# Optimization experiments

Measured on AMD Instinct MI355X. Metric: run time of the kernel, lower is better.

The kernel has to match this reference:

```python
import jax, jax.numpy as jnp
import numpy as np

N_NODES = 2000
N_FEAT = 16
HID = 64
RNN_LAYERS = 2
OUT_WIN = 24
OUT_DIM = 1
N_Q = 3
LN_EPS = 1e-5


def _layernorm(x, g, b):
    mu = jnp.mean(x, axis=-1, keepdims=True)
    var = jnp.mean((x - mu) ** 2, axis=-1, keepdims=True)
    return (x - mu) * jax.lax.rsqrt(var + LN_EPS) * g + b


def setup_inputs() -> dict:
    key = jax.random.key(0)
    ks = jax.random.split(key, 24)
    B, S, N, F, H = 4, 96, N_NODES, N_FEAT, HID
    E = 16000
    inp = {}
    inp['x'] = jax.random.normal(ks[0], (B, S, N, F), dtype=jnp.float32)
    inp['edge_index'] = jax.random.randint(ks[1], (2, E), 0, N, dtype=jnp.int64)
    inp['edge_weight'] = jax.random.uniform(ks[2], (E,), dtype=jnp.float32)
    sc = 1.0 / np.sqrt(H)
    inp['W_gcn'] = jax.random.normal(ks[3], (H, F)) * (1.0 / np.sqrt(F))
    inp['b_gcn'] = jnp.zeros((H,))
    inp['Wq'] = jax.random.normal(ks[4], (H, H)) * sc
    inp['Wk'] = jax.random.normal(ks[5], (H, H)) * sc
    inp['Wv'] = jax.random.normal(ks[6], (H, H)) * sc
    inp['v_w'] = jax.random.normal(ks[7], (1, H)) * sc
    inp['v_b'] = jnp.zeros((1,))
    inp['ln1_g'] = jnp.ones((H,)); inp['ln1_b'] = jnp.zeros((H,))
    inp['gru_Wih'] = jax.random.normal(ks[8], (RNN_LAYERS, 3 * H, H)) * sc
    inp['gru_Whh'] = jax.random.normal(ks[9], (RNN_LAYERS, 3 * H, H)) * sc
    inp['gru_bih'] = jnp.zeros((RNN_LAYERS, 3 * H))
    inp['gru_bhh'] = jnp.zeros((RNN_LAYERS, 3 * H))
    inp['ln2_g'] = jnp.ones((H,)); inp['ln2_b'] = jnp.zeros((H,))
    inp['pre1_W'] = jax.random.normal(ks[10], (2 * H, H)) * sc
    inp['pre1_b'] = jnp.zeros((2 * H,))
    inp['pre2_W'] = jax.random.normal(ks[11], (N * H, 2 * H)) * (1.0 / np.sqrt(2 * H))
    inp['pre2_b'] = jnp.zeros((N * H,))
    inp['low_W'] = jax.random.normal(ks[12], (OUT_WIN * OUT_DIM, H)) * sc
    inp['low_b'] = jnp.zeros((OUT_WIN * OUT_DIM,))
    inp['inc_W'] = jax.random.normal(ks[13], (OUT_WIN * OUT_DIM * (N_Q - 1), H)) * sc
    inp['inc_b'] = jnp.zeros((OUT_WIN * OUT_DIM * (N_Q - 1),))
    return inp


def reference(x, edge_index, edge_weight, W_gcn, b_gcn, Wq, Wk, Wv, v_w, v_b,
              ln1_g, ln1_b, gru_Wih, gru_Whh, gru_bih, gru_bhh, ln2_g, ln2_b,
              pre1_W, pre1_b, pre2_W, pre2_b, low_W, low_b, inc_W, inc_b):
    B, S, N, F = x.shape
    H = W_gcn.shape[0]
    # ---- GCNConv (PyG semantics: add self-loops, symmetric normalization) ----
    # Graph is identical across batch/timesteps, so vectorize the per-timestep
    # loop into one batched gather/scatter.
    src, dst = edge_index[0], edge_index[1]
    loops = jnp.arange(N, dtype=edge_index.dtype)
    src_a = jnp.concatenate([src, loops])
    dst_a = jnp.concatenate([dst, loops])
    ew_a = jnp.concatenate([edge_weight, jnp.ones((N,), dtype=edge_weight.dtype)])
    deg = jax.ops.segment_sum(ew_a, dst_a, num_segments=N)
    dinv = jnp.where(deg > 0, deg ** -0.5, 0.0)
    coef = dinv[src_a] * ew_a * dinv[dst_a]  # (E+N,)
    xw = jnp.einsum('bsnf,hf->bsnh', x, W_gcn)  # linear (no bias yet)
    msg = xw[:, :, src_a, :] * coef[None, None, :, None]  # (B,S,E+N,H)
    h = jnp.zeros((B, S, N, H), dtype=xw.dtype).at[:, :, dst_a].add(msg)
    h = jax.nn.elu(h + b_gcn)  # dropout is identity in eval
    # ---- additive attention over all (t, node) positions ----
    keys = h.reshape(B, S * N, H)
    query = h[:, -1].mean(axis=1)  # (B,H)
    qp = query @ Wq.T  # (B,H)
    kp = keys @ Wk.T   # (B,SN,H)
    vp = keys @ Wv.T
    energy = jnp.tanh(qp[:, None, :] + kp)
    scores = energy @ v_w[0] + v_b[0]  # (B,SN)
    attn = jax.nn.softmax(scores, axis=1)
    context = jnp.einsum('bk,bkh->bh', attn, vp)
    context = _layernorm(context, ln1_g, ln1_b)
    # ---- GRU with seq_len=1, h0=0 (torch gate order: r,z,n) ----
    inp = context
    for l in range(gru_Wih.shape[0]):
        gi = inp @ gru_Wih[l].T + gru_bih[l]  # (B,3H)
        gh = gru_bhh[l]                        # h_prev = 0
        i_r, i_z, i_n = jnp.split(gi, 3, axis=-1)
        h_r, h_z, h_n = jnp.split(gh, 3, axis=-1)
        r = jax.nn.sigmoid(i_r + h_r)
        z = jax.nn.sigmoid(i_z + h_z)
        n = jnp.tanh(i_n + r * h_n)
        inp = (1.0 - z) * n  # + z * 0
    final = _layernorm(inp, ln2_g, ln2_b)
    # ---- pre_head -> per-node features ----
    f = jax.nn.elu(final @ pre1_W.T + pre1_b)
    nf = (f @ pre2_W.T + pre2_b).reshape(B, N, H)
    # ---- monotonic quantile head ----
    q_low = (nf @ low_W.T + low_b).reshape(B, N, OUT_WIN, OUT_DIM)
    inc = jax.nn.softplus((nf @ inc_W.T + inc_b).reshape(B, N, OUT_WIN, OUT_DIM, N_Q - 1))
    q1 = q_low + inc[..., 0]
    q2 = q1 + inc[..., 1]
    quant = jnp.stack([q_low, q1, q2], axis=-1)  # (B,N,OW,OD,Q)
    predictions = jnp.transpose(quant, (0, 2, 1, 3, 4))  # (B,OW,N,OD,Q)
    return predictions, attn.reshape(B, S, N)
```

## Files before the change

### kernel.cpp

```cpp
#include <hip/hip_runtime.h>

#define B 4
#define S 96
#define NN 2000
#define FF 16
#define HH 64
#define EE 16000
#define SN (S*NN)
#define SLICES (B*S)
#define BSN (B*SN)
#define KB_TOTAL (BSN/16)
#define KB_PER_B (SN/16)
#define OUT_PRED (B*24*NN*3)

typedef __attribute__((ext_vector_type(8))) short short8;
typedef __attribute__((ext_vector_type(4))) float f32x4;

__device__ __forceinline__ unsigned short f2bf(float f){
  unsigned u = __float_as_uint(f);
  u += 0x7fffu + ((u >> 16) & 1u);
  return (unsigned short)(u >> 16);
}
__device__ __forceinline__ float bf2f(unsigned short s){
  return __uint_as_float(((unsigned)s) << 16);
}
__device__ __forceinline__ float fast_tanh(float x){
  float e = __builtin_amdgcn_exp2f(x * 2.8853900817779268f);
  return 1.0f - 2.0f * __builtin_amdgcn_rcpf(e + 1.0f);
}
__device__ __forceinline__ float sigm(float x){ return 1.0f / (1.0f + __expf(-x)); }
__device__ __forceinline__ float eluf(float x){ return x > 0.0f ? x : expm1f(x); }
__device__ __forceinline__ float softplusf_(float x){
  return fmaxf(x, 0.0f) + log1pf(__expf(-fabsf(x)));
}

__global__ void k_pinit(float* __restrict__ degw, int* __restrict__ cnt){
  int i = blockIdx.x * 256 + threadIdx.x;
  if (i < NN){ degw[i] = 1.0f; cnt[i] = 1; }
}

__global__ void k_deg(const int* __restrict__ ei, const float* __restrict__ ew,
                      float* __restrict__ degw, int* __restrict__ cnt){
  int e = blockIdx.x * 256 + threadIdx.x;
  if (e < EE){
    int d = ei[EE + e];
    atomicAdd(&degw[d], ew[e]);
    atomicAdd(&cnt[d], 1);
  }
}

__global__ void k_scan(const int* __restrict__ cnt, float* __restrict__ degw,
                       int* __restrict__ rowptr, int* __restrict__ curs){
  __shared__ int tsum[256];
  int tid = threadIdx.x;
  for (int i = tid; i < NN; i += 256){
    float deg = degw[i];
    degw[i] = deg > 0.0f ? rsqrtf(deg) : 0.0f;
  }
  int base = tid * 8;
  int loc[8]; int s = 0;
  #pragma unroll
  for (int j = 0; j < 8; ++j){
    int v = (base + j < NN) ? cnt[base + j] : 0;
    loc[j] = s; s += v;
  }
  tsum[tid] = s;
  __syncthreads();
  for (int off = 1; off < 256; off <<= 1){
    int v = (tid >= off) ? tsum[tid - off] : 0;
    __syncthreads();
    tsum[tid] += v;
    __syncthreads();
  }
  int excl = tsum[tid] - s;
  #pragma unroll
  for (int j = 0; j < 8; ++j)
    if (base + j < NN){ rowptr[base + j] = excl + loc[j]; curs[base + j] = excl + loc[j]; }
  if (tid == 0) rowptr[NN] = EE + NN;
}

__global__ void k_fill(const int* __restrict__ ei, const float* __restrict__ ew,
                       const float* __restrict__ dinv, int* __restrict__ curs,
                       uint2* __restrict__ epack){
  int e = blockIdx.x * 256 + threadIdx.x;
  if (e < EE){
    int s0 = ei[e], d = ei[EE + e];
    int pos = atomicAdd(&curs[d], 1);
    epack[pos] = make_uint2((unsigned)s0, __float_as_uint(dinv[s0] * ew[e] * dinv[d]));
  }
  int i = blockIdx.x * 256 + threadIdx.x;
  if (i < NN){
    int pos = atomicAdd(&curs[i], 1);
    epack[pos] = make_uint2((unsigned)i, __float_as_uint(dinv[i] * dinv[i]));
  }
}

__global__ __launch_bounds__(512) void k_agg(const float* __restrict__ x,
    const int* __restrict__ rowptr, const uint2* __restrict__ epack,
    unsigned* __restrict__ aggG){
  __shared__ unsigned xs[2][NN * 4];
  int tid = threadIdx.x;
  int spair = blockIdx.x >> 1;
  int halfF = blockIdx.x & 1;
  int s0 = spair * 2;

  #pragma unroll
  for (int ss = 0; ss < 2; ++ss){
    const float* xg = x + (size_t)(s0 + ss) * (NN * FF) + halfF * 8;
    for (int i = tid; i < 4000; i += 512){
      int n = i >> 1, p = i & 1;
      float4 v = *(const float4*)(xg + n * 16 + p * 4);
      xs[ss][n * 4 + p * 2]     = (unsigned)f2bf(v.x) | ((unsigned)f2bf(v.y) << 16);
      xs[ss][n * 4 + p * 2 + 1] = (unsigned)f2bf(v.z) | ((unsigned)f2bf(v.w) << 16);
    }
  }
  __syncthreads();

  int rs[4], re[4];
  #pragma unroll
  for (int g = 0; g < 4; ++g){
    int n = g * 512 + tid;
    if (n < NN){ rs[g] = rowptr[n]; re[g] = rowptr[n + 1]; }
    else { rs[g] = 0; re[g] = 0; }
  }
  float agg[4][2][8];
  #pragma unroll
  for (int g = 0; g < 4; ++g)
    #pragma unroll
    for (int ss = 0; ss < 2; ++ss)
      #pragma unroll
      for (int i = 0; i < 8; ++i) agg[g][ss][i] = 0.0f;

  #pragma unroll
  for (int g = 0; g < 4; ++g){
    for (int e = rs[g]; e < re[g]; ++e){
      uint2 m = epack[e];
      int s = (int)m.x;
      float c = __uint_as_float(m.y);
      uint4 u0 = *(const uint4*)&xs[0][s * 4];
      uint4 u1 = *(const uint4*)&xs[1][s * 4];
      agg[g][0][0] += c * __uint_as_float(u0.x << 16);
      agg[g][0][1] += c * __uint_as_float(u0.x & 0xffff0000u);
      agg[g][0][2] += c * __uint_as_float(u0.y << 16);
      agg[g][0][3] += c * __uint_as_float(u0.y & 0xffff0000u);
      agg[g][0][4] += c * __uint_as_float(u0.z << 16);
      agg[g][0][5] += c * __uint_as_float(u0.z & 0xffff0000u);
      agg[g][0][6] += c * __uint_as_float(u0.w << 16);
      agg[g][0][7] += c * __uint_as_float(u0.w & 0xffff0000u);
      agg[g][1][0] += c * __uint_as_float(u1.x << 16);
      agg[g][1][1] += c * __uint_as_float(u1.x & 0xffff0000u);
      agg[g][1][2] += c * __uint_as_float(u1.y << 16);
      agg[g][1][3] += c * __uint_as_float(u1.y & 0xffff0000u);
      agg[g][1][4] += c * __uint_as_float(u1.z << 16);
      agg[g][1][5] += c * __uint_as_float(u1.z & 0xffff0000u);
      agg[g][1][6] += c * __uint_as_float(u1.w << 16);
      agg[g][1][7] += c * __uint_as_float(u1.w & 0xffff0000u);
    }
  }
  #pragma unroll
  for (int g = 0; g < 4; ++g){
    int n = g * 512 + tid;
    if (n < NN){
      #pragma unroll
      for (int ss = 0; ss < 2; ++ss){
        unsigned u[4];
        #pragma unroll
        for (int j = 0; j < 4; ++j)
          u[j] = (unsigned)f2bf(agg[g][ss][2*j]) | ((unsigned)f2bf(agg[g][ss][2*j+1]) << 16);
        uint4* dst = (uint4*)(aggG + ((size_t)(s0 + ss) * NN + n) * 8 + halfF * 4);
        *dst = make_uint4(u[0], u[1], u[2], u[3]);
      }
    }
  }
}

__global__ __launch_bounds__(256) void k_xform(const unsigned short* __restrict__ aggG,
    const float* __restrict__ Wg, const float* __restrict__ bg,
    unsigned short* __restrict__ h){
  int lane = threadIdx.x & 63;
  int wid  = threadIdx.x >> 6;
  int wgid = blockIdx.x * 4 + wid;
  int row16 = lane & 15, half = lane >> 4;

  short8 bf[4];
  #pragma unroll
  for (int t = 0; t < 4; ++t){
    short8 v;
    #pragma unroll
    for (int j = 0; j < 8; ++j) v[j] = 0;
    if (half < 2){
      const float* wr = Wg + (t * 16 + row16) * 16 + half * 8;
      #pragma unroll
      for (int j = 0; j < 8; ++j) v[j] = (short)f2bf(wr[j]);
    }
    bf[t] = v;
  }
  float bias[4];
  #pragma unroll
  for (int t = 0; t < 4; ++t) bias[t] = bg[t * 16 + row16];

  for (int nb = wgid; nb < KB_TOTAL; nb += 8192){
    short8 af;
    #pragma unroll
    for (int j = 0; j < 8; ++j) af[j] = 0;
    if (half < 2)
      af = *(const short8*)(aggG + ((size_t)nb * 16 + row16) * 16 + half * 8);

    f32x4 acc[4];
    #pragma unroll
    for (int t = 0; t < 4; ++t){
      f32x4 a = {0.f, 0.f, 0.f, 0.f};
      acc[t] = __builtin_amdgcn_mfma_f32_16x16x32_bf16(af, bf[t], a, 0, 0, 0);
    }
    unsigned short* hp = h + (size_t)nb * 16 * 64;
    #pragma unroll
    for (int t = 0; t < 4; ++t){
      #pragma unroll
      for (int r = 0; r < 4; ++r){
        float v = acc[t][r] + bias[t];
        float e = v > 0.0f ? v : __expf(v) - 1.0f;
        hp[(half * 4 + r) * 64 + t * 16 + row16] = f2bf(e);
      }
    }
  }
}

__global__ void k_query(const unsigned short* __restrict__ h,
                        const float* __restrict__ Wq, float* __restrict__ qp){
  __shared__ float part[256];
  __shared__ float q[64];
  int b = blockIdx.x, tid = threadIdx.x;
  int i = tid & 63, chunk = tid >> 6;
  const unsigned short* hb = h + ((size_t)(b * S + (S - 1)) * NN) * HH;
  float p = 0.0f;
  for (int n = chunk * 500; n < chunk * 500 + 500; ++n) p += bf2f(hb[n * HH + i]);
  part[tid] = p;
  __syncthreads();
  if (tid < 64) q[tid] = (part[tid] + part[tid+64] + part[tid+128] + part[tid+192]) * (1.0f / NN);
  __syncthreads();
  if (tid < 64){
    float acc = 0.0f;
    for (int k = 0; k < 64; ++k) acc += q[k] * Wq[tid * 64 + k];
    qp[b * 64 + tid] = acc;
  }
}

__global__ __launch_bounds__(256) void k_scores(const unsigned short* __restrict__ h,
    const float* __restrict__ Wk, const float* __restrict__ vw,
    const float* __restrict__ qp, float* __restrict__ scores){
  int lane = threadIdx.x & 63;
  int wid = threadIdx.x >> 6;
  int wgid = blockIdx.x * 4 + wid;
  int row16 = lane & 15, half = lane >> 4;

  short8 bf[4][2];
  #pragma unroll
  for (int t = 0; t < 4; ++t){
    int n = 16 * t + row16;
    #pragma unroll
    for (int s2 = 0; s2 < 2; ++s2){
      const float* wr = Wk + n * 64 + 32 * s2 + half * 8;
      short8 v;
      #pragma unroll
      for (int j = 0; j < 8; ++j) v[j] = (short)f2bf(wr[j]);
      bf[t][s2] = v;
    }
  }
  float vwv[4];
  #pragma unroll
  for (int t = 0; t < 4; ++t) vwv[t] = vw[16 * t + row16];

  int b = wgid / 2000;
  float qv[4];
  #pragma unroll
  for (int t = 0; t < 4; ++t) qv[t] = qp[b * 64 + 16 * t + row16];

  int kb0 = wgid * 6;
  #pragma unroll 2
  for (int i = 0; i < 6; ++i){
    int kb = kb0 + i;
    const short* hp = (const short*)h + (size_t)kb * 16 * 64;
    short8 af[2];
    #pragma unroll
    for (int s2 = 0; s2 < 2; ++s2)
      af[s2] = *(const short8*)(hp + row16 * 64 + 32 * s2 + half * 8);

    f32x4 acc[4];
    #pragma unroll
    for (int t = 0; t < 4; ++t){
      f32x4 a = {0.f, 0.f, 0.f, 0.f};
      a = __builtin_amdgcn_mfma_f32_16x16x32_bf16(af[0], bf[t][0], a, 0, 0, 0);
      a = __builtin_amdgcn_mfma_f32_16x16x32_bf16(af[1], bf[t][1], a, 0, 0, 0);
      acc[t] = a;
    }
    float part[4] = {0, 0, 0, 0};
    #pragma unroll
    for (int t = 0; t < 4; ++t){
      #pragma unroll
      for (int r = 0; r < 4; ++r)
        part[r] += vwv[t] * fast_tanh(qv[t] + acc[t][r]);
    }
    #pragma unroll
    for (int r = 0; r < 4; ++r){
      part[r] += __shfl_xor(part[r], 1);
      part[r] += __shfl_xor(part[r], 2);
      part[r] += __shfl_xor(part[r], 4);
      part[r] += __shfl_xor(part[r], 8);
    }
    if (row16 == 0){
      #pragma unroll
      for (int r = 0; r < 4; ++r) scores[kb * 16 + half * 4 + r] = part[r];
    }
  }
}

__global__ void k_smax1(const float* __restrict__ scores, float* __restrict__ part2){
  __shared__ float red[256];
  int b = blockIdx.x >> 7, blk = blockIdx.x & 127, tid = threadIdx.x;
  const float* sc = scores + (size_t)b * SN + blk * 1500;
  float m = -1e30f;
  for (int k = tid; k < 1500; k += 256) m = fmaxf(m, sc[k]);
  red[tid] = m; __syncthreads();
  for (int s2 = 128; s2 > 0; s2 >>= 1){
    if (tid < s2) red[tid] = fmaxf(red[tid], red[tid + s2]);
    __syncthreads();
  }
  float bm = red[0]; __syncthreads();
  float sum = 0.f;
  for (int k = tid; k < 1500; k += 256) sum += __expf(sc[k] - bm);
  red[tid] = sum; __syncthreads();
  for (int s2 = 128; s2 > 0; s2 >>= 1){
    if (tid < s2) red[tid] += red[tid + s2];
    __syncthreads();
  }
  if (tid == 0){
    part2[(b * 128 + blk) * 2]     = bm;
    part2[(b * 128 + blk) * 2 + 1] = red[0];
  }
}

__global__ void k_smax2(const float* __restrict__ part2, float* __restrict__ Msum){
  int b = threadIdx.x;
  if (b < B){
    float M = -1e30f;
    for (int i = 0; i < 128; ++i) M = fmaxf(M, part2[(b * 128 + i) * 2]);
    float Ssum = 0.f;
    for (int i = 0; i < 128; ++i)
      Ssum += part2[(b * 128 + i) * 2 + 1] * __expf(part2[(b * 128 + i) * 2] - M);
    Msum[b] = M;
    Msum[4 + b] = 1.0f / Ssum;
  }
}

__global__ __launch_bounds__(256) void k_ctx(const float* __restrict__ scores,
    const float* __restrict__ Msum, const unsigned short* __restrict__ h,
    float* __restrict__ ctx_raw, float* __restrict__ outp){
  __shared__ float red[4 * 64];
  int lane = threadIdx.x & 63, wid = threadIdx.x >> 6;
  int b = blockIdx.x >> 7;
  int blk = blockIdx.x & 127;
  int kr = lane >> 3, fb = lane & 7;
  float M = Msum[b], Si = Msum[4 + b];
  const float* sc = scores + (size_t)b * SN;
  const unsigned short* hb = h + (size_t)b * SN * 64;
  float* ao = outp + OUT_PRED + (size_t)b * SN;

  float acc[8];
  #pragma unroll
  for (int j = 0; j < 8; ++j) acc[j] = 0.0f;

  for (int k0 = (blk * 4 + wid) * 8; k0 < SN; k0 += 4096){
    int k = k0 + kr;
    float a = __expf(sc[k] - M) * Si;
    uint4 u = *(const uint4*)(hb + (size_t)k * 64 + fb * 8);
    if (fb == 0) ao[k] = a;
    acc[0] += a * __uint_as_float(u.x << 16);
    acc[1] += a * __uint_as_float(u.x & 0xffff0000u);
    acc[2] += a * __uint_as_float(u.y << 16);
    acc[3] += a * __uint_as_float(u.y & 0xffff0000u);
    acc[4] += a * __uint_as_float(u.z << 16);
    acc[5] += a * __uint_as_float(u.z & 0xffff0000u);
    acc[6] += a * __uint_as_float(u.w << 16);
    acc[7] += a * __uint_as_float(u.w & 0xffff0000u);
  }
  #pragma unroll
  for (int j = 0; j < 8; ++j){
    acc[j] += __shfl_xor(acc[j], 8);
    acc[j] += __shfl_xor(acc[j], 16);
    acc[j] += __shfl_xor(acc[j], 32);
  }
  if (kr == 0){
    #pragma unroll
    for (int j = 0; j < 8; ++j) red[wid * 64 + fb * 8 + j] = acc[j];
  }
  __syncthreads();
  if (wid == 0){
    float t = red[lane] + red[64 + lane] + red[128 + lane] + red[192 + lane];
    atomicAdd(&ctx_raw[b * 64 + lane], t);
  }
}

__global__ void k_head(const float* __restrict__ ctx_raw, const float* __restrict__ Wv,
    const float* __restrict__ ln1g, const float* __restrict__ ln1b,
    const float* __restrict__ Wih, const float* __restrict__ bih,
    const float* __restrict__ bhh,
    const float* __restrict__ ln2g, const float* __restrict__ ln2b,
    const float* __restrict__ pre1W, const float* __restrict__ pre1b,
    float* __restrict__ fout){
  __shared__ float cr[64], vec[64], stat[2];
  int b = blockIdx.x, t = threadIdx.x;
  if (t < 64) cr[t] = ctx_raw[b * 64 + t];
  __syncthreads();
  float c = 0.f;
  if (t < 64){
    for (int i = 0; i < 64; ++i) c += cr[i] * Wv[t * 64 + i];
  }
  __syncthreads();
  if (t < 64) vec[t] = c;
  __syncthreads();
  if (t == 0){
    float mu = 0; for (int i = 0; i < 64; ++i) mu += vec[i]; mu *= (1.f/64.f);
    float va = 0; for (int i = 0; i < 64; ++i){ float d = vec[i] - mu; va += d * d; }
    va *= (1.f/64.f);
    stat[0] = mu; stat[1] = rsqrtf(va + 1e-5f);
  }
  __syncthreads();
  if (t < 64) cr[t] = (vec[t] - stat[0]) * stat[1] * ln1g[t] + ln1b[t];
  __syncthreads();
  for (int l = 0; l < 2; ++l){
    float nv = 0.f;
    if (t < 64){
      const float* W = Wih + l * 192 * 64;
      const float* bi = bih + l * 192;
      const float* bh = bhh + l * 192;
      float ir = bi[t], iz = bi[64 + t], in_ = bi[128 + t];
      for (int i = 0; i < 64; ++i){
        float v = cr[i];
        ir  += v * W[t * 64 + i];
        iz  += v * W[(64 + t) * 64 + i];
        in_ += v * W[(128 + t) * 64 + i];
      }
      float r = sigm(ir + bh[t]);
      float z = sigm(iz + bh[64 + t]);
      float nn2 = fast_tanh(in_ + r * bh[128 + t]);
      nv = (1.0f - z) * nn2;
    }
    __syncthreads();
    if (t < 64) cr[t] = nv;
    __syncthreads();
  }
  if (t == 0){
    float mu = 0; for (int i = 0; i < 64; ++i) mu += cr[i]; mu *= (1.f/64.f);
    float va = 0; for (int i = 0; i < 64; ++i){ float d = cr[i] - mu; va += d * d; }
    va *= (1.f/64.f);
    stat[0] = mu; stat[1] = rsqrtf(va + 1e-5f);
  }
  __syncthreads();
  if (t < 64) vec[t] = (cr[t] - stat[0]) * stat[1] * ln2g[t] + ln2b[t];
  __syncthreads();
  float fc = pre1b[t];
  for (int j = 0; j < 64; ++j) fc += vec[j] * pre1W[t * 64 + j];
  fout[b * 128 + t] = eluf(fc);
}

__global__ __launch_bounds__(256) void k_out(const float* __restrict__ f_g,
    const float* __restrict__ pre2W, const float* __restrict__ pre2b,
    const float* __restrict__ lowW, const float* __restrict__ lowb,
    const float* __restrict__ incW, const float* __restrict__ incb,
    float* __restrict__ outp){
  __shared__ float w72T[64 * 72];
  __shared__ float nf_lds[4][64 * 4];
  int tid = threadIdx.x;
  int lane = tid & 63, wid = tid >> 6;
  int row16 = lane & 15, half = lane >> 4;

  for (int i = tid; i < 64 * 72; i += 256){
    int j = i / 72, o = i - j * 72;
    w72T[i] = (o < 24) ? lowW[o * 64 + j] : incW[(o - 24) * 64 + j];
  }

  short8 bfr[4];
  #pragma unroll
  for (int s = 0; s < 4; ++s){
    short8 v;
    #pragma unroll
    for (int j = 0; j < 8; ++j) v[j] = 0;
    if (row16 < 4){
      const float* fr = f_g + row16 * 128 + s * 32 + half * 8;
      #pragma unroll
      for (int j = 0; j < 8; ++j) v[j] = (short)f2bf(fr[j]);
    }
    bfr[s] = v;
  }
  __syncthreads();

  int n = blockIdx.x * 4 + wid;
  float* nfw = &nf_lds[wid][0];
  #pragma unroll
  for (int rb = 0; rb < 4; ++rb){
    f32x4 acc = {0.f, 0.f, 0.f, 0.f};
    #pragma unroll
    for (int s = 0; s < 4; ++s){
      const float* ar = pre2W + ((size_t)(n * 64 + rb * 16 + row16)) * 128 + s * 32 + half * 8;
      short8 av;
      #pragma unroll
      for (int j = 0; j < 8; ++j) av[j] = (short)f2bf(ar[j]);
      acc = __builtin_amdgcn_mfma_f32_16x16x32_bf16(av, bfr[s], acc, 0, 0, 0);
    }
    if (row16 < 4){
      #pragma unroll
      for (int r = 0; r < 4; ++r){
        int j = rb * 16 + half * 4 + r;
        nfw[j * 4 + row16] = acc[r] + pre2b[n * 64 + j];
      }
    }
  }
  __syncthreads();

  #pragma unroll
  for (int rnd = 0; rnd < 2; ++rnd){
    int wo = rnd * 16 + (lane >> 2);
    int b = lane & 3;
    if (wo < 24){
      float q0 = lowb[wo], i0 = incb[2 * wo], i1 = incb[2 * wo + 1];
      #pragma unroll 4
      for (int j = 0; j < 64; ++j){
        float v = nfw[j * 4 + b];
        q0 += v * w72T[j * 72 + wo];
        i0 += v * w72T[j * 72 + 24 + 2 * wo];
        i1 += v * w72T[j * 72 + 24 + 2 * wo + 1];
      }
      float p0 = q0;
      float p1 = p0 + softplusf_(i0);
      float p2 = p1 + softplusf_(i1);
      size_t ob = ((size_t)(b * 24 + wo) * NN + n) * 3;
      outp[ob] = p0; outp[ob + 1] = p1; outp[ob + 2] = p2;
    }
  }
}

extern "C" void kernel_launch(void* const* d_in, const int* in_sizes, int n_in,
                              void* d_out, int out_size, void* d_ws, size_t ws_size,
                              hipStream_t stream){
  const float* x     = (const float*)d_in[0];
  const int*   ei    = (const int*)d_in[1];
  const float* ew    = (const float*)d_in[2];
  const float* Wg    = (const float*)d_in[3];
  const float* bg    = (const float*)d_in[4];
  const float* Wq    = (const float*)d_in[5];
  const float* Wk    = (const float*)d_in[6];
  const float* Wv    = (const float*)d_in[7];
  const float* vw    = (const float*)d_in[8];
  const float* ln1g  = (const float*)d_in[10];
  const float* ln1b  = (const float*)d_in[11];
  const float* Wih   = (const float*)d_in[12];
  const float* bih   = (const float*)d_in[14];
  const float* bhh   = (const float*)d_in[15];
  const float* ln2g  = (const float*)d_in[16];
  const float* ln2b  = (const float*)d_in[17];
  const float* pre1W = (const float*)d_in[18];
  const float* pre1b = (const float*)d_in[19];
  const float* pre2W = (const float*)d_in[20];
  const float* pre2b = (const float*)d_in[21];
  const float* lowW  = (const float*)d_in[22];
  const float* lowb  = (const float*)d_in[23];
  const float* incW  = (const float*)d_in[24];
  const float* incb  = (const float*)d_in[25];
  float* outp = (float*)d_out;

  char* ws = (char*)d_ws;
  size_t off = 0;
  auto alloc = [&](size_t bytes) -> char* {
    char* p = ws + off;
    off += (bytes + 255) & ~(size_t)255;
    return p;
  };
  unsigned short* h  = (unsigned short*)alloc((size_t)BSN * 64 * 2);
  unsigned* aggG     = (unsigned*)alloc((size_t)BSN * 8 * 4);
  float* scores      = (float*)alloc((size_t)BSN * 4);
  int*   rowptr      = (int*)alloc((NN + 1) * 4);
  uint2* epack       = (uint2*)alloc((EE + NN) * 8);
  float* degw        = (float*)alloc(NN * 4);
  int*   cnt         = (int*)alloc(NN * 4);
  int*   curs        = (int*)alloc(NN * 4);
  float* qp          = (float*)alloc(B * 64 * 4);
  float* part2       = (float*)alloc(B * 128 * 2 * 4);
  float* Msum        = (float*)alloc(8 * 4);
  float* ctx_raw     = (float*)alloc(B * 64 * 4);
  float* f_g         = (float*)alloc(B * 128 * 4);
  (void)ws_size; (void)in_sizes; (void)n_in; (void)out_size;

  (void)hipMemsetAsync(ctx_raw, 0, B * 64 * 4, stream);
  k_pinit <<<(NN + 255) / 256, 256, 0, stream>>>(degw, cnt);
  k_deg   <<<(EE + 255) / 256, 256, 0, stream>>>(ei, ew, degw, cnt);
  k_scan  <<<1, 256, 0, stream>>>(cnt, degw, rowptr, curs);
  k_fill  <<<(EE + 255) / 256, 256, 0, stream>>>(ei, ew, degw, curs, epack);
  k_agg   <<<SLICES, 512, 0, stream>>>(x, rowptr, epack, aggG);
  k_xform <<<2048, 256, 0, stream>>>((const unsigned short*)aggG, Wg, bg, h);
  k_query <<<B, 256, 0, stream>>>(h, Wq, qp);
  k_scores<<<2000, 256, 0, stream>>>(h, Wk, vw, qp, scores);
  k_smax1 <<<512, 256, 0, stream>>>(scores, part2);
  k_smax2 <<<1, 64, 0, stream>>>(part2, Msum);
  k_ctx   <<<512, 256, 0, stream>>>(scores, Msum, h, ctx_raw, outp);
  k_head  <<<B, 128, 0, stream>>>(ctx_raw, Wv, ln1g, ln1b, Wih, bih, bhh,
                                  ln2g, ln2b, pre1W, pre1b, f_g);
  k_out   <<<500, 256, 0, stream>>>(f_g, pre2W, pre2b, lowW, lowb, incW, incb, outp);
}
```

Before: 220.8 us.

## Recompute GCN transform in context kernel instead of reading materialized h

The attention-context kernel no longer reads the 64-wide bf16 hidden tensor h. It recomputes h from the 16-wide aggregated features with MFMA, bias and ELU, applying the same bf16 rounding as before. This cuts global reads in k_ctx roughly fourfold, at the cost of extra MFMA and exp work. The grid is also re-split to 1000 blocks, each covering 12 fixed 16-row chunks, instead of the strided loop.

```diff
diff --git a/kernel.cpp b/kernel.cpp
--- a/kernel.cpp
+++ b/kernel.cpp
@@ -353,50 +353,83 @@
 }
 
 __global__ __launch_bounds__(256) void k_ctx(const float* __restrict__ scores,
-    const float* __restrict__ Msum, const unsigned short* __restrict__ h,
+    const float* __restrict__ Msum, const unsigned short* __restrict__ aggG,
+    const float* __restrict__ Wg, const float* __restrict__ bg,
     float* __restrict__ ctx_raw, float* __restrict__ outp){
   __shared__ float red[4 * 64];
   int lane = threadIdx.x & 63, wid = threadIdx.x >> 6;
-  int b = blockIdx.x >> 7;
-  int blk = blockIdx.x & 127;
-  int kr = lane >> 3, fb = lane & 7;
+  int wgid = blockIdx.x * 4 + wid;
+  int row16 = lane & 15, half = lane >> 4;
+
+  short8 bf[4];
+  #pragma unroll
+  for (int t = 0; t < 4; ++t){
+    short8 v;
+    #pragma unroll
+    for (int j = 0; j < 8; ++j) v[j] = 0;
+    if (half < 2){
+      const float* wr = Wg + (t * 16 + row16) * 16 + half * 8;
+      #pragma unroll
+      for (int j = 0; j < 8; ++j) v[j] = (short)f2bf(wr[j]);
+    }
+    bf[t] = v;
+  }
+  float bias[4];
+  #pragma unroll
+  for (int t = 0; t < 4; ++t) bias[t] = bg[t * 16 + row16];
+
+  int b = wgid / 1000;
   float M = Msum[b], Si = Msum[4 + b];
-  const float* sc = scores + (size_t)b * SN;
-  const unsigned short* hb = h + (size_t)b * SN * 64;
-  float* ao = outp + OUT_PRED + (size_t)b * SN;
-
-  float acc[8];
-  #pragma unroll
-  for (int j = 0; j < 8; ++j) acc[j] = 0.0f;
-
-  for (int k0 = (blk * 4 + wid) * 8; k0 < SN; k0 += 4096){
-    int k = k0 + kr;
-    float a = __expf(sc[k] - M) * Si;
-    uint4 u = *(const uint4*)(hb + (size_t)k * 64 + fb * 8);
-    if (fb == 0) ao[k] = a;
-    acc[0] += a * __uint_as_float(u.x << 16);
-    acc[1] += a * __uint_as_float(u.x & 0xffff0000u);
-    acc[2] += a * __uint_as_float(u.y << 16);
-    acc[3] += a * __uint_as_float(u.y & 0xffff0000u);
-    acc[4] += a * __uint_as_float(u.z << 16);
-    acc[5] += a * __uint_as_float(u.z & 0xffff0000u);
-    acc[6] += a * __uint_as_float(u.w << 16);
-    acc[7] += a * __uint_as_float(u.w & 0xffff0000u);
-  }
-  #pragma unroll
-  for (int j = 0; j < 8; ++j){
-    acc[j] += __shfl_xor(acc[j], 8);
-    acc[j] += __shfl_xor(acc[j], 16);
-    acc[j] += __shfl_xor(acc[j], 32);
-  }
-  if (kr == 0){
-    #pragma unroll
-    for (int j = 0; j < 8; ++j) red[wid * 64 + fb * 8 + j] = acc[j];
+  float* ao = outp + OUT_PRED;
+
+  float acc4[4] = {0.f, 0.f, 0.f, 0.f};
+  int kb0 = wgid * 12;
+  for (int i = 0; i < 12; ++i){
+    int kb = kb0 + i;
+    short8 af;
+    #pragma unroll
+    for (int j = 0; j < 8; ++j) af[j] = 0;
+    if (half < 2)
+      af = *(const short8*)(aggG + ((size_t)kb * 16 + row16) * 16 + half * 8);
+
+    f32x4 hz[4];
+    #pragma unroll
+    for (int t = 0; t < 4; ++t){
+      f32x4 a = {0.f, 0.f, 0.f, 0.f};
+      hz[t] = __builtin_amdgcn_mfma_f32_16x16x32_bf16(af, bf[t], a, 0, 0, 0);
+    }
+    float ar[4];
+    #pragma unroll
+    for (int r = 0; r < 4; ++r)
+      ar[r] = __expf(scores[kb * 16 + half * 4 + r] - M) * Si;
+    if (row16 == 0){
+      #pragma unroll
+      for (int r = 0; r < 4; ++r) ao[kb * 16 + half * 4 + r] = ar[r];
+    }
+    #pragma unroll
+    for (int t = 0; t < 4; ++t){
+      #pragma unroll
+      for (int r = 0; r < 4; ++r){
+        float v = hz[t][r] + bias[t];
+        float e = v > 0.0f ? v : __expf(v) - 1.0f;
+        e = __uint_as_float(((unsigned)f2bf(e)) << 16);
+        acc4[t] += ar[r] * e;
+      }
+    }
+  }
+  #pragma unroll
+  for (int t = 0; t < 4; ++t){
+    acc4[t] += __shfl_xor(acc4[t], 16);
+    acc4[t] += __shfl_xor(acc4[t], 32);
+  }
+  if (half == 0){
+    #pragma unroll
+    for (int t = 0; t < 4; ++t) red[wid * 64 + t * 16 + row16] = acc4[t];
   }
   __syncthreads();
   if (wid == 0){
-    float t = red[lane] + red[64 + lane] + red[128 + lane] + red[192 + lane];
-    atomicAdd(&ctx_raw[b * 64 + lane], t);
+    float tsum = red[lane] + red[64 + lane] + red[128 + lane] + red[192 + lane];
+    atomicAdd(&ctx_raw[b * 64 + lane], tsum);
   }
 }
 
@@ -601,7 +634,8 @@
   k_scores<<<2000, 256, 0, stream>>>(h, Wk, vw, qp, scores);
   k_smax1 <<<512, 256, 0, stream>>>(scores, part2);
   k_smax2 <<<1, 64, 0, stream>>>(part2, Msum);
-  k_ctx   <<<512, 256, 0, stream>>>(scores, Msum, h, ctx_raw, outp);
+  k_ctx   <<<1000, 256, 0, stream>>>(scores, Msum, (const unsigned short*)aggG, Wg, bg,
+                                     ctx_raw, outp);
   k_head  <<<B, 128, 0, stream>>>(ctx_raw, Wv, ln1g, ln1b, Wih, bih, bhh,
                                   ln2g, ln2b, pre1W, pre1b, f_g);
   k_out   <<<500, 256, 0, stream>>>(f_g, pre2W, pre2b, lowW, lowb, incW, incb, outp);
```

New measurement: 225.4 us. +2.0%, slower.
